# Kernel optimization log

Hardware: AMD Instinct MI355X
Metric: run time of the kernel (lower is better)

Reference implementation:

```python
import jax, jax.numpy as jnp
import numpy as np

N = 100000
E = 1600000
IN_DIM, HIDDEN, OUT_DIM, HEADS = 256, 128, 64, 2
NEG_SLOPE = 0.2


def setup_inputs() -> dict:
    key = jax.random.key(0)
    ks = jax.random.split(key, 10)
    inv = lambda d: 1.0 / np.sqrt(d)
    return {
        "x": jax.random.normal(ks[0], (N, IN_DIM), dtype=jnp.float32),
        "edge_index": jax.random.randint(ks[1], (2, E), 0, N, dtype=jnp.int64),
        "W1": jax.random.normal(ks[2], (IN_DIM, HEADS * HIDDEN), dtype=jnp.float32) * inv(IN_DIM),
        "att_src1": jax.random.normal(ks[3], (HEADS, HIDDEN), dtype=jnp.float32) * inv(HIDDEN),
        "att_dst1": jax.random.normal(ks[4], (HEADS, HIDDEN), dtype=jnp.float32) * inv(HIDDEN),
        "b1": jnp.zeros((HIDDEN,), dtype=jnp.float32),
        "W2": jax.random.normal(ks[5], (HIDDEN, OUT_DIM), dtype=jnp.float32) * inv(HIDDEN),
        "att_src2": jax.random.normal(ks[6], (1, OUT_DIM), dtype=jnp.float32) * inv(OUT_DIM),
        "att_dst2": jax.random.normal(ks[7], (1, OUT_DIM), dtype=jnp.float32) * inv(OUT_DIM),
        "b2": jnp.zeros((OUT_DIM,), dtype=jnp.float32),
    }


def gat_conv(x, W, att_src, att_dst, bias, src, dst, heads, ch):
    # Linear transform: [N, H, C]
    h = (x @ W).reshape(N, heads, ch)
    # Per-node attention logits: [N, H]
    a_s = jnp.einsum("nhc,hc->nh", h, att_src)
    a_d = jnp.einsum("nhc,hc->nh", h, att_dst)
    # Edge-wise scores (self-loops already in src/dst): [E', H]
    e = jax.nn.leaky_relu(a_s[src] + a_d[dst], NEG_SLOPE)
    # Segment softmax over incoming edges of each dst node
    m = jax.ops.segment_max(e, dst, num_segments=N)
    alpha = jnp.exp(e - m[dst])
    denom = jax.ops.segment_sum(alpha, dst, num_segments=N)
    alpha = alpha / denom[dst]
    # Weighted scatter-add aggregation: [N, H, C]
    out = jax.ops.segment_sum(alpha[:, :, None] * h[src], dst, num_segments=N)
    # concat=False -> mean over heads, then bias
    return out.mean(axis=1) + bias


def reference(x, edge_index, W1, att_src1, att_dst1, b1, W2, att_src2, att_dst2, b2):
    # PyG GATConv default: add self-loops
    loop = jnp.arange(N, dtype=edge_index.dtype)
    src = jnp.concatenate([edge_index[0], loop])
    dst = jnp.concatenate([edge_index[1], loop])
    h = gat_conv(x, W1, att_src1, att_dst1, b1, src, dst, HEADS, HIDDEN)
    h = jax.nn.relu(h)  # dropout is identity in eval mode
    out = gat_conv(h, W2, att_src2, att_dst2, b2, src, dst, 1, OUT_DIM)
    return out
```

## Files before the change

kernel.cpp:

```cpp
#include <hip/hip_runtime.h>
#include <hip/hip_bf16.h>
#include <cstdint>
#include <cstddef>

#define IN_D 256
#define HID 128
#define OUT_D 64
#define NSLOPE 0.2f
#define PAD 128
#define CSTR 16

typedef __attribute__((ext_vector_type(8))) short bf16x8;
typedef __attribute__((ext_vector_type(4))) float f32x4;
typedef __attribute__((ext_vector_type(8))) unsigned short u16x8;
typedef unsigned short u16;

static inline int cdiv(long long a, long long b) { return (int)((a + b - 1) / b); }

__device__ __forceinline__ float lrelu(float v) { return v >= 0.f ? v : NSLOPE * v; }

__device__ __forceinline__ u16 f2bf(float f) {
  unsigned u = __float_as_uint(f);
  return (u16)((u + 0x7FFFu + ((u >> 16) & 1u)) >> 16);
}
__device__ __forceinline__ float bf2f(u16 h) {
  return __uint_as_float((unsigned)h << 16);
}

__global__ void k_prep(const float* __restrict__ W1, u16* __restrict__ WThi,
                       u16* __restrict__ WTlo, const float* __restrict__ W2,
                       u16* __restrict__ W2Thi, u16* __restrict__ W2Tlo) {
  int idx = blockIdx.x * 256 + threadIdx.x;
  if (idx < IN_D * IN_D) {
    int k = idx >> 8, n = idx & 255;
    float f = W1[idx];
    u16 h = f2bf(f);
    WThi[n * IN_D + k] = h;
    WTlo[n * IN_D + k] = f2bf(f - bf2f(h));
  }
  int idx2 = idx - IN_D * IN_D;
  if (idx2 >= 0 && idx2 < HID * OUT_D) {
    int k = idx2 >> 6, n = idx2 & 63;
    float f = W2[idx2];
    u16 h = f2bf(f);
    W2Thi[n * HID + k] = h;
    W2Tlo[n * HID + k] = f2bf(f - bf2f(h));
  }
}

__launch_bounds__(512)
__global__ void k_gemm1buck(const float* __restrict__ x, const u16* __restrict__ WThi,
                            const u16* __restrict__ WTlo,
                            const float* __restrict__ as1, const float* __restrict__ ad1,
                            u16* __restrict__ hb, float* __restrict__ a_s,
                            float* __restrict__ a_d, int N,
                            const int* __restrict__ ei, int E,
                            int* __restrict__ cnt, int* __restrict__ colp,
                            int G1, int G2) {
  __shared__ u16 ldsb[2][10240];
  int bid = blockIdx.x;
  int m2 = (G1 < G2 ? G1 : G2) * 2;
  int type, tb;
  if (bid < m2) { type = bid & 1; tb = bid >> 1; }
  else { int ex = bid - m2; type = (G1 > G2) ? 0 : 1; tb = m2 / 2 + ex; }

  if (type == 1) {
    int base = tb * 2048 + threadIdx.x;
    int sv[4], dv[4]; bool vv[4];
    #pragma unroll
    for (int q = 0; q < 4; ++q) {
      int i = base + q * 512;
      vv[q] = i < E;
      int ic = vv[q] ? i : 0;
      sv[q] = ei[ic];
      dv[q] = ei[E + ic];
    }
    int pv[4];
    #pragma unroll
    for (int q = 0; q < 4; ++q)
      pv[q] = vv[q] ? atomicAdd(&cnt[(size_t)dv[q] * CSTR], 1) : PAD;
    #pragma unroll
    for (int q = 0; q < 4; ++q)
      if (pv[q] < PAD) colp[(size_t)dv[q] * PAD + pv[q]] = sv[q];
    return;
  }

  int tid = threadIdx.x;
  int w = tid >> 6, l = tid & 63;
  int l15 = l & 15, l4 = l >> 4;
  int rowbase = tb * 128 + w * 16;
  int row = rowbase + l15;
  int rowc = (row < N) ? row : (N - 1);
  const float* xp = x + (size_t)rowc * IN_D + l4 * 8;

  f32x4 acc[16];
  #pragma unroll
  for (int t = 0; t < 16; ++t) acc[t] = (f32x4){0.f, 0.f, 0.f, 0.f};

  const int ridx = (l15 * 5 + l4) * 8;

  for (int kk = 0; kk < 8; ++kk) {
    __syncthreads();
    #pragma unroll
    for (int it = 0; it < 2; ++it) {
      int c = tid + it * 512;
      int n = c >> 2, ch = c & 3;
      size_t soff = (size_t)n * IN_D + kk * 32 + ch * 8;
      uint4 vh = *(const uint4*)(WThi + soff);
      uint4 vl = *(const uint4*)(WTlo + soff);
      int dsl = (n * 5 + ch) * 8;
      *(uint4*)&ldsb[0][dsl] = vh;
      *(uint4*)&ldsb[1][dsl] = vl;
    }
    __syncthreads();

    f32x4 v0 = *(const f32x4*)(xp + kk * 32);
    f32x4 v1 = *(const f32x4*)(xp + kk * 32 + 4);
    bf16x8 ah, al;
    #pragma unroll
    for (int j = 0; j < 4; ++j) {
      u16 h0 = f2bf(v0[j]);
      ah[j] = (short)h0; al[j] = (short)f2bf(v0[j] - bf2f(h0));
      u16 h1 = f2bf(v1[j]);
      ah[j + 4] = (short)h1; al[j + 4] = (short)f2bf(v1[j] - bf2f(h1));
    }
    #pragma unroll
    for (int t = 0; t < 16; ++t) {
      bf16x8 bh = *(const bf16x8*)&ldsb[0][ridx + t * 640];
      bf16x8 bl = *(const bf16x8*)&ldsb[1][ridx + t * 640];
      acc[t] = __builtin_amdgcn_mfma_f32_16x16x32_bf16(ah, bh, acc[t], 0, 0, 0);
      acc[t] = __builtin_amdgcn_mfma_f32_16x16x32_bf16(al, bh, acc[t], 0, 0, 0);
      acc[t] = __builtin_amdgcn_mfma_f32_16x16x32_bf16(ah, bl, acc[t], 0, 0, 0);
    }
  }

  #pragma unroll
  for (int r = 0; r < 4; ++r) {
    int rr = rowbase + l4 * 4 + r;
    if (rr < N) {
      u16* hp = hb + (size_t)rr * IN_D + l15;
      #pragma unroll
      for (int t = 0; t < 16; ++t) hp[t * 16] = f2bf(acc[t][r]);
    }
  }
  float asv[16], adv[16];
  #pragma unroll
  for (int t = 0; t < 16; ++t) { asv[t] = as1[t * 16 + l15]; adv[t] = ad1[t * 16 + l15]; }
  float ps0[4] = {}, ps1[4] = {}, pd0[4] = {}, pd1[4] = {};
  #pragma unroll
  for (int t = 0; t < 16; ++t) {
    #pragma unroll
    for (int r = 0; r < 4; ++r) {
      float v = acc[t][r];
      if (t < 8) { ps0[r] += v * asv[t]; pd0[r] += v * adv[t]; }
      else       { ps1[r] += v * asv[t]; pd1[r] += v * adv[t]; }
    }
  }
  #pragma unroll
  for (int r = 0; r < 4; ++r) {
    #pragma unroll
    for (int o = 1; o < 16; o <<= 1) {
      ps0[r] += __shfl_xor(ps0[r], o); ps1[r] += __shfl_xor(ps1[r], o);
      pd0[r] += __shfl_xor(pd0[r], o); pd1[r] += __shfl_xor(pd1[r], o);
    }
    int rr = rowbase + l4 * 4 + r;
    if (l15 == 0 && rr < N) {
      a_s[rr * 2] = ps0[r]; a_s[rr * 2 + 1] = ps1[r];
      a_d[rr * 2] = pd0[r]; a_d[rr * 2 + 1] = pd1[r];
    }
  }
}

__launch_bounds__(256)
__global__ void k_fagg1(const int* __restrict__ cnt, const int* __restrict__ colp,
                        const float* __restrict__ a_s, const float* __restrict__ a_d,
                        const u16* __restrict__ hb, float* __restrict__ aggm, int N) {
  int gid = blockIdx.x * blockDim.x + threadIdx.x;
  int n = gid >> 6, lane = gid & 63;
  if (n >= N) return;
  size_t beg = (size_t)n * PAD;
  int cn = cnt[(size_t)n * CSTR]; cn = (cn < PAD) ? cn : PAD;
  float ad0 = a_d[2 * n], ad1 = a_d[2 * n + 1];

  int half = lane >> 5;
  int l5 = lane & 31;
  int head = l5 >> 4;
  float myAd = head ? ad1 : ad0;

  float sacc = 0.f;
  float accv[8] = {};
  if (half == 0) {
    float2 asn = *(const float2*)&a_s[2 * (size_t)n];
    float w = __expf(lrelu((head ? asn.y : asn.x) + myAd));
    sacc = w;
    const u16x8 hv = *(const u16x8*)&hb[(size_t)n * IN_D + l5 * 8];
    #pragma unroll
    for (int q = 0; q < 8; ++q) accv[q] = w * bf2f(hv[q]);
  }
  #pragma unroll 4
  for (int j = 0; j < cn; j += 2) {
    int jj = j + half;
    bool valid = jj < cn;
    int jc = valid ? jj : 0;
    int sidx = colp[beg + jc];
    float2 asv = *(const float2*)&a_s[2 * (size_t)sidx];
    float e = (head ? asv.y : asv.x) + myAd;
    float w = __expf(lrelu(e));
    w = valid ? w : 0.f;
    sacc += w;
    const u16x8 hv = *(const u16x8*)&hb[(size_t)sidx * IN_D + l5 * 8];
    #pragma unroll
    for (int q = 0; q < 8; ++q) accv[q] += w * bf2f(hv[q]);
  }
  sacc += __shfl_xor(sacc, 32);
  float myScale = 0.5f / sacc;
  #pragma unroll
  for (int q = 0; q < 8; ++q) {
    accv[q] *= myScale;
    accv[q] += __shfl_xor(accv[q], 16);
    accv[q] += __shfl_xor(accv[q], 32);
  }
  if (lane < 16) {
    float4 o0 = {accv[0], accv[1], accv[2], accv[3]};
    float4 o1 = {accv[4], accv[5], accv[6], accv[7]};
    *(float4*)&aggm[(size_t)n * HID + lane * 8] = o0;
    *(float4*)&aggm[(size_t)n * HID + lane * 8 + 4] = o1;
  }
}

__launch_bounds__(256)
__global__ void k_gemm2(const float* __restrict__ aggm, const float* __restrict__ b1,
                        const u16* __restrict__ WThi, const u16* __restrict__ WTlo,
                        const float* __restrict__ as2, const float* __restrict__ ad2,
                        u16* __restrict__ h2b, float* __restrict__ a_s,
                        float* __restrict__ a_d, int N) {
  int tid = threadIdx.x;
  int w = tid >> 6, l = tid & 63;
  int l15 = l & 15, l4 = l >> 4;
  int rowbase = blockIdx.x * 64 + w * 16;
  int row = rowbase + l15;
  int rowc = (row < N) ? row : (N - 1);
  const float* ap = aggm + (size_t)rowc * HID + l4 * 8;
  const float* bp = b1 + l4 * 8;

  f32x4 acc[4];
  #pragma unroll
  for (int t = 0; t < 4; ++t) acc[t] = (f32x4){0.f, 0.f, 0.f, 0.f};

  #pragma unroll
  for (int kk = 0; kk < 4; ++kk) {
    f32x4 v0 = *(const f32x4*)(ap + kk * 32);
    f32x4 v1 = *(const f32x4*)(ap + kk * 32 + 4);
    f32x4 b0 = *(const f32x4*)(bp + kk * 32);
    f32x4 b1v = *(const f32x4*)(bp + kk * 32 + 4);
    bf16x8 ah, al;
    #pragma unroll
    for (int j = 0; j < 4; ++j) {
      float u0 = v0[j] + b0[j]; u0 = (u0 > 0.f) ? u0 : 0.f;
      u16 h0 = f2bf(u0);
      ah[j] = (short)h0; al[j] = (short)f2bf(u0 - bf2f(h0));
      float u1 = v1[j] + b1v[j]; u1 = (u1 > 0.f) ? u1 : 0.f;
      u16 h1 = f2bf(u1);
      ah[j + 4] = (short)h1; al[j + 4] = (short)f2bf(u1 - bf2f(h1));
    }
    size_t boff = (size_t)l15 * HID + kk * 32 + l4 * 8;
    #pragma unroll
    for (int t = 0; t < 4; ++t) {
      bf16x8 bh = *(const bf16x8*)(WThi + boff + (size_t)t * 16 * HID);
      bf16x8 bl = *(const bf16x8*)(WTlo + boff + (size_t)t * 16 * HID);
      acc[t] = __builtin_amdgcn_mfma_f32_16x16x32_bf16(ah, bh, acc[t], 0, 0, 0);
      acc[t] = __builtin_amdgcn_mfma_f32_16x16x32_bf16(al, bh, acc[t], 0, 0, 0);
      acc[t] = __builtin_amdgcn_mfma_f32_16x16x32_bf16(ah, bl, acc[t], 0, 0, 0);
    }
  }

  #pragma unroll
  for (int r = 0; r < 4; ++r) {
    int rr = rowbase + l4 * 4 + r;
    if (rr < N) {
      u16* hp = h2b + (size_t)rr * OUT_D + l15;
      #pragma unroll
      for (int t = 0; t < 4; ++t) hp[t * 16] = f2bf(acc[t][r]);
    }
  }
  float asv[4], adv[4];
  #pragma unroll
  for (int t = 0; t < 4; ++t) { asv[t] = as2[t * 16 + l15]; adv[t] = ad2[t * 16 + l15]; }
  #pragma unroll
  for (int r = 0; r < 4; ++r) {
    float ps = 0.f, pd = 0.f;
    #pragma unroll
    for (int t = 0; t < 4; ++t) { ps += acc[t][r] * asv[t]; pd += acc[t][r] * adv[t]; }
    #pragma unroll
    for (int o = 1; o < 16; o <<= 1) { ps += __shfl_xor(ps, o); pd += __shfl_xor(pd, o); }
    int rr = rowbase + l4 * 4 + r;
    if (l15 == 0 && rr < N) { a_s[rr] = ps; a_d[rr] = pd; }
  }
}

__launch_bounds__(256)
__global__ void k_fagg2(const int* __restrict__ cnt, const int* __restrict__ colp,
                        const float* __restrict__ a_s, const float* __restrict__ a_d,
                        const u16* __restrict__ h2b, const float* __restrict__ b2,
                        float* __restrict__ out, int N) {
  int gid = blockIdx.x * blockDim.x + threadIdx.x;
  int n = gid >> 6, lane = gid & 63;
  if (n >= N) return;
  size_t beg = (size_t)n * PAD;
  int cn = cnt[(size_t)n * CSTR]; cn = (cn < PAD) ? cn : PAD;
  float ad = a_d[n];

  int g = lane >> 3, l3 = lane & 7;
  float sacc = 0.f;
  float accv[8] = {};
  if (g == 0) {
    float w = __expf(lrelu(a_s[n] + ad));
    sacc = w;
    const u16x8 hv = *(const u16x8*)&h2b[(size_t)n * OUT_D + l3 * 8];
    #pragma unroll
    for (int q = 0; q < 8; ++q) accv[q] = w * bf2f(hv[q]);
  }
  #pragma unroll 4
  for (int j = 0; j < cn; j += 8) {
    int jj = j + g;
    bool valid = jj < cn;
    int jc = valid ? jj : 0;
    int sidx = colp[beg + jc];
    float w = __expf(lrelu(a_s[sidx] + ad));
    w = valid ? w : 0.f;
    sacc += w;
    const u16x8 hv = *(const u16x8*)&h2b[(size_t)sidx * OUT_D + l3 * 8];
    #pragma unroll
    for (int q = 0; q < 8; ++q) accv[q] += w * bf2f(hv[q]);
  }
  sacc += __shfl_xor(sacc, 8);
  sacc += __shfl_xor(sacc, 16);
  sacc += __shfl_xor(sacc, 32);
  float rcp = 1.f / sacc;
  #pragma unroll
  for (int q = 0; q < 8; ++q) {
    accv[q] *= rcp;
    accv[q] += __shfl_xor(accv[q], 8);
    accv[q] += __shfl_xor(accv[q], 16);
    accv[q] += __shfl_xor(accv[q], 32);
  }
  if (lane < 8) {
    float* op = out + (size_t)n * OUT_D + lane * 8;
    const float* bp = b2 + lane * 8;
    float4 o0 = {accv[0] + bp[0], accv[1] + bp[1], accv[2] + bp[2], accv[3] + bp[3]};
    float4 o1 = {accv[4] + bp[4], accv[5] + bp[5], accv[6] + bp[6], accv[7] + bp[7]};
    *(float4*)op = o0;
    *(float4*)(op + 4) = o1;
  }
}

extern "C" void kernel_launch(void* const* d_in, const int* in_sizes, int n_in,
                              void* d_out, int out_size, void* d_ws, size_t ws_size,
                              hipStream_t stream) {
  const float* x    = (const float*)d_in[0];
  const int*   ei   = (const int*)d_in[1];
  const float* W1   = (const float*)d_in[2];
  const float* as1w = (const float*)d_in[3];
  const float* ad1w = (const float*)d_in[4];
  const float* b1   = (const float*)d_in[5];
  const float* W2   = (const float*)d_in[6];
  const float* as2w = (const float*)d_in[7];
  const float* ad2w = (const float*)d_in[8];
  const float* b2   = (const float*)d_in[9];
  float* out = (float*)d_out;

  const int N  = in_sizes[0] / IN_D;
  const int E  = in_sizes[1] / 2;

  float* ws = (float*)d_ws;
  size_t off = 0;
  u16*   hb1  = (u16*)(ws + off); off += (size_t)N * IN_D / 2;
  u16*   h2b  = (u16*)(ws + off); off += (size_t)N * OUT_D / 2;
  float* aggm = ws + off; off += (size_t)N * HID;
  float* a_s1 = ws + off; off += (size_t)N * 2;
  float* a_d1 = ws + off; off += (size_t)N * 2;
  float* a_s2 = ws + off; off += N;
  float* a_d2 = ws + off; off += N;
  int*   cnt  = (int*)(ws + off); off += (size_t)N * CSTR;
  int*   colp = (int*)(ws + off); off += (size_t)N * PAD;
  u16*   WThi = (u16*)(ws + off); off += (IN_D * IN_D) / 2;
  u16*   WTlo = (u16*)(ws + off); off += (IN_D * IN_D) / 2;
  u16*   W2Thi = (u16*)(ws + off); off += (HID * OUT_D) / 2;
  u16*   W2Tlo = (u16*)(ws + off); off += (HID * OUT_D) / 2;

  hipMemsetAsync(cnt, 0, (size_t)N * CSTR * sizeof(int), stream);

  k_prep<<<cdiv(IN_D * IN_D + HID * OUT_D, 256), 256, 0, stream>>>(
      W1, WThi, WTlo, W2, W2Thi, W2Tlo);

  const int G1 = cdiv(N, 128);
  const int G2 = cdiv(E, 2048);
  k_gemm1buck<<<G1 + G2, 512, 0, stream>>>(x, WThi, WTlo, as1w, ad1w, hb1, a_s1, a_d1, N,
                                           ei, E, cnt, colp, G1, G2);

  k_fagg1<<<cdiv((long long)N * 64, 256), 256, 0, stream>>>(cnt, colp, a_s1, a_d1, hb1, aggm, N);

  k_gemm2<<<cdiv(N, 64), 256, 0, stream>>>(aggm, b1, W2Thi, W2Tlo, as2w, ad2w, h2b, a_s2, a_d2, N);
  k_fagg2<<<cdiv((long long)N * 64, 256), 256, 0, stream>>>(cnt, colp, a_s2, a_d2, h2b, b2, out, N);
}
```

Baseline: 374.5 us.

## Fuse layer-1 aggregation with layer-2 GEMM and compact degree counters

```diff
diff --git a/kernel.cpp b/kernel.cpp
--- a/kernel.cpp
+++ b/kernel.cpp
@@ -8,7 +8,6 @@
 #define OUT_D 64
 #define NSLOPE 0.2f
 #define PAD 128
-#define CSTR 16
 
 typedef __attribute__((ext_vector_type(8))) short bf16x8;
 typedef __attribute__((ext_vector_type(4))) float f32x4;
@@ -78,7 +77,7 @@
     int pv[4];
     #pragma unroll
     for (int q = 0; q < 4; ++q)
-      pv[q] = vv[q] ? atomicAdd(&cnt[(size_t)dv[q] * CSTR], 1) : PAD;
+      pv[q] = vv[q] ? atomicAdd(&cnt[dv[q]], 1) : PAD;
     #pragma unroll
     for (int q = 0; q < 4; ++q)
       if (pv[q] < PAD) colp[(size_t)dv[q] * PAD + pv[q]] = sv[q];
@@ -172,129 +171,116 @@
 }
 
 __launch_bounds__(256)
-__global__ void k_fagg1(const int* __restrict__ cnt, const int* __restrict__ colp,
-                        const float* __restrict__ a_s, const float* __restrict__ a_d,
-                        const u16* __restrict__ hb, float* __restrict__ aggm, int N) {
-  int gid = blockIdx.x * blockDim.x + threadIdx.x;
-  int n = gid >> 6, lane = gid & 63;
-  if (n >= N) return;
-  size_t beg = (size_t)n * PAD;
-  int cn = cnt[(size_t)n * CSTR]; cn = (cn < PAD) ? cn : PAD;
-  float ad0 = a_d[2 * n], ad1 = a_d[2 * n + 1];
+__global__ void k_fagg1g2(const int* __restrict__ cnt, const int* __restrict__ colp,
+                          const float* __restrict__ a_s, const float* __restrict__ a_d,
+                          const u16* __restrict__ hb, const float* __restrict__ b1,
+                          const u16* __restrict__ W2Thi, const u16* __restrict__ W2Tlo,
+                          const float* __restrict__ as2, const float* __restrict__ ad2,
+                          u16* __restrict__ h2b, float* __restrict__ a_s2,
+                          float* __restrict__ a_d2, int N) {
+  __shared__ float rowLds[16][132];
+  __shared__ float red[2][16][4];
+  int tid = threadIdx.x;
+  int wid = tid >> 6, lane = tid & 63;
+  int base = blockIdx.x * 16;
 
   int half = lane >> 5;
   int l5 = lane & 31;
   int head = l5 >> 4;
-  float myAd = head ? ad1 : ad0;
-
-  float sacc = 0.f;
-  float accv[8] = {};
-  if (half == 0) {
-    float2 asn = *(const float2*)&a_s[2 * (size_t)n];
-    float w = __expf(lrelu((head ? asn.y : asn.x) + myAd));
-    sacc = w;
-    const u16x8 hv = *(const u16x8*)&hb[(size_t)n * IN_D + l5 * 8];
-    #pragma unroll
-    for (int q = 0; q < 8; ++q) accv[q] = w * bf2f(hv[q]);
-  }
-  #pragma unroll 4
-  for (int j = 0; j < cn; j += 2) {
-    int jj = j + half;
-    bool valid = jj < cn;
-    int jc = valid ? jj : 0;
-    int sidx = colp[beg + jc];
-    float2 asv = *(const float2*)&a_s[2 * (size_t)sidx];
-    float e = (head ? asv.y : asv.x) + myAd;
-    float w = __expf(lrelu(e));
-    w = valid ? w : 0.f;
-    sacc += w;
-    const u16x8 hv = *(const u16x8*)&hb[(size_t)sidx * IN_D + l5 * 8];
-    #pragma unroll
-    for (int q = 0; q < 8; ++q) accv[q] += w * bf2f(hv[q]);
-  }
-  sacc += __shfl_xor(sacc, 32);
-  float myScale = 0.5f / sacc;
-  #pragma unroll
-  for (int q = 0; q < 8; ++q) {
-    accv[q] *= myScale;
-    accv[q] += __shfl_xor(accv[q], 16);
-    accv[q] += __shfl_xor(accv[q], 32);
-  }
-  if (lane < 16) {
-    float4 o0 = {accv[0], accv[1], accv[2], accv[3]};
-    float4 o1 = {accv[4], accv[5], accv[6], accv[7]};
-    *(float4*)&aggm[(size_t)n * HID + lane * 8] = o0;
-    *(float4*)&aggm[(size_t)n * HID + lane * 8 + 4] = o1;
-  }
-}
-
-__launch_bounds__(256)
-__global__ void k_gemm2(const float* __restrict__ aggm, const float* __restrict__ b1,
-                        const u16* __restrict__ WThi, const u16* __restrict__ WTlo,
-                        const float* __restrict__ as2, const float* __restrict__ ad2,
-                        u16* __restrict__ h2b, float* __restrict__ a_s,
-                        float* __restrict__ a_d, int N) {
-  int tid = threadIdx.x;
-  int w = tid >> 6, l = tid & 63;
-  int l15 = l & 15, l4 = l >> 4;
-  int rowbase = blockIdx.x * 64 + w * 16;
-  int row = rowbase + l15;
-  int rowc = (row < N) ? row : (N - 1);
-  const float* ap = aggm + (size_t)rowc * HID + l4 * 8;
-  const float* bp = b1 + l4 * 8;
-
-  f32x4 acc[4];
-  #pragma unroll
-  for (int t = 0; t < 4; ++t) acc[t] = (f32x4){0.f, 0.f, 0.f, 0.f};
-
+
+  for (int rr = 0; rr < 4; ++rr) {
+    int ln = wid * 4 + rr;
+    int n = base + ln;
+    if (n >= N) { if (lane < 16) for (int q = 0; q < 8; ++q) rowLds[ln][lane * 8 + q] = 0.f; continue; }
+    size_t begb = (size_t)n * PAD;
+    int cn = cnt[n]; cn = (cn < PAD) ? cn : PAD;
+    float ad0 = a_d[2 * n], ad1 = a_d[2 * n + 1];
+    float myAd = head ? ad1 : ad0;
+
+    float sacc = 0.f;
+    float accv[8] = {};
+    if (half == 0) {
+      float2 asn = *(const float2*)&a_s[2 * (size_t)n];
+      float wv = __expf(lrelu((head ? asn.y : asn.x) + myAd));
+      sacc = wv;
+      const u16x8 hv = *(const u16x8*)&hb[(size_t)n * IN_D + l5 * 8];
+      #pragma unroll
+      for (int q = 0; q < 8; ++q) accv[q] = wv * bf2f(hv[q]);
+    }
+    #pragma unroll 4
+    for (int j = 0; j < cn; j += 2) {
+      int jj = j + half;
+      bool valid = jj < cn;
+      int jc = valid ? jj : 0;
+      int sidx = colp[begb + jc];
+      float2 asv = *(const float2*)&a_s[2 * (size_t)sidx];
+      float e = (head ? asv.y : asv.x) + myAd;
+      float wv = __expf(lrelu(e));
+      wv = valid ? wv : 0.f;
+      sacc += wv;
+      const u16x8 hv = *(const u16x8*)&hb[(size_t)sidx * IN_D + l5 * 8];
+      #pragma unroll
+      for (int q = 0; q < 8; ++q) accv[q] += wv * bf2f(hv[q]);
+    }
+    sacc += __shfl_xor(sacc, 32);
+    float myScale = 0.5f / sacc;
+    #pragma unroll
+    for (int q = 0; q < 8; ++q) {
+      accv[q] *= myScale;
+      accv[q] += __shfl_xor(accv[q], 16);
+      accv[q] += __shfl_xor(accv[q], 32);
+    }
+    if (lane < 16) {
+      #pragma unroll
+      for (int q = 0; q < 8; ++q) rowLds[ln][lane * 8 + q] = accv[q];
+    }
+  }
+  __syncthreads();
+
+  int l15 = lane & 15, l4 = lane >> 4;
+  f32x4 acc2 = (f32x4){0.f, 0.f, 0.f, 0.f};
   #pragma unroll
   for (int kk = 0; kk < 4; ++kk) {
-    f32x4 v0 = *(const f32x4*)(ap + kk * 32);
-    f32x4 v1 = *(const f32x4*)(ap + kk * 32 + 4);
-    f32x4 b0 = *(const f32x4*)(bp + kk * 32);
-    f32x4 b1v = *(const f32x4*)(bp + kk * 32 + 4);
+    int k0 = kk * 32 + l4 * 8;
+    f32x4 bv0 = *(const f32x4*)(b1 + k0);
+    f32x4 bv1 = *(const f32x4*)(b1 + k0 + 4);
     bf16x8 ah, al;
     #pragma unroll
     for (int j = 0; j < 4; ++j) {
-      float u0 = v0[j] + b0[j]; u0 = (u0 > 0.f) ? u0 : 0.f;
+      float u0 = rowLds[l15][k0 + j] + bv0[j]; u0 = (u0 > 0.f) ? u0 : 0.f;
       u16 h0 = f2bf(u0);
       ah[j] = (short)h0; al[j] = (short)f2bf(u0 - bf2f(h0));
-      float u1 = v1[j] + b1v[j]; u1 = (u1 > 0.f) ? u1 : 0.f;
+      float u1 = rowLds[l15][k0 + 4 + j] + bv1[j]; u1 = (u1 > 0.f) ? u1 : 0.f;
       u16 h1 = f2bf(u1);
       ah[j + 4] = (short)h1; al[j + 4] = (short)f2bf(u1 - bf2f(h1));
     }
-    size_t boff = (size_t)l15 * HID + kk * 32 + l4 * 8;
-    #pragma unroll
-    for (int t = 0; t < 4; ++t) {
-      bf16x8 bh = *(const bf16x8*)(WThi + boff + (size_t)t * 16 * HID);
-      bf16x8 bl = *(const bf16x8*)(WTlo + boff + (size_t)t * 16 * HID);
-      acc[t] = __builtin_amdgcn_mfma_f32_16x16x32_bf16(ah, bh, acc[t], 0, 0, 0);
-      acc[t] = __builtin_amdgcn_mfma_f32_16x16x32_bf16(al, bh, acc[t], 0, 0, 0);
-      acc[t] = __builtin_amdgcn_mfma_f32_16x16x32_bf16(ah, bl, acc[t], 0, 0, 0);
-    }
-  }
-
+    size_t boff = (size_t)(wid * 16 + l15) * HID + k0;
+    bf16x8 bh = *(const bf16x8*)(W2Thi + boff);
+    bf16x8 bl = *(const bf16x8*)(W2Tlo + boff);
+    acc2 = __builtin_amdgcn_mfma_f32_16x16x32_bf16(ah, bh, acc2, 0, 0, 0);
+    acc2 = __builtin_amdgcn_mfma_f32_16x16x32_bf16(al, bh, acc2, 0, 0, 0);
+    acc2 = __builtin_amdgcn_mfma_f32_16x16x32_bf16(ah, bl, acc2, 0, 0, 0);
+  }
+
+  float asv = as2[wid * 16 + l15], adv = ad2[wid * 16 + l15];
+  float ps[4], pd[4];
   #pragma unroll
   for (int r = 0; r < 4; ++r) {
-    int rr = rowbase + l4 * 4 + r;
-    if (rr < N) {
-      u16* hp = h2b + (size_t)rr * OUT_D + l15;
-      #pragma unroll
-      for (int t = 0; t < 4; ++t) hp[t * 16] = f2bf(acc[t][r]);
-    }
-  }
-  float asv[4], adv[4];
-  #pragma unroll
-  for (int t = 0; t < 4; ++t) { asv[t] = as2[t * 16 + l15]; adv[t] = ad2[t * 16 + l15]; }
-  #pragma unroll
-  for (int r = 0; r < 4; ++r) {
-    float ps = 0.f, pd = 0.f;
-    #pragma unroll
-    for (int t = 0; t < 4; ++t) { ps += acc[t][r] * asv[t]; pd += acc[t][r] * adv[t]; }
-    #pragma unroll
-    for (int o = 1; o < 16; o <<= 1) { ps += __shfl_xor(ps, o); pd += __shfl_xor(pd, o); }
-    int rr = rowbase + l4 * 4 + r;
-    if (l15 == 0 && rr < N) { a_s[rr] = ps; a_d[rr] = pd; }
+    int n = base + l4 * 4 + r;
+    if (n < N) h2b[(size_t)n * OUT_D + wid * 16 + l15] = f2bf(acc2[r]);
+    ps[r] = acc2[r] * asv; pd[r] = acc2[r] * adv;
+    #pragma unroll
+    for (int o = 1; o < 16; o <<= 1) { ps[r] += __shfl_xor(ps[r], o); pd[r] += __shfl_xor(pd[r], o); }
+    if (l15 == 0) { red[0][l4 * 4 + r][wid] = ps[r]; red[1][l4 * 4 + r][wid] = pd[r]; }
+  }
+  __syncthreads();
+  if (tid < 32) {
+    int ln = tid >> 1, kind = tid & 1;
+    int n = base + ln;
+    if (n < N) {
+      float v = red[kind][ln][0] + red[kind][ln][1] + red[kind][ln][2] + red[kind][ln][3];
+      if (kind == 0) a_s2[n] = v; else a_d2[n] = v;
+    }
   }
 }
 
@@ -307,7 +293,7 @@
   int n = gid >> 6, lane = gid & 63;
   if (n >= N) return;
   size_t beg = (size_t)n * PAD;
-  int cn = cnt[(size_t)n * CSTR]; cn = (cn < PAD) ? cn : PAD;
+  int cn = cnt[n]; cn = (cn < PAD) ? cn : PAD;
   float ad = a_d[n];
 
   int g = lane >> 3, l3 = lane & 7;
@@ -376,19 +362,18 @@
   size_t off = 0;
   u16*   hb1  = (u16*)(ws + off); off += (size_t)N * IN_D / 2;
   u16*   h2b  = (u16*)(ws + off); off += (size_t)N * OUT_D / 2;
-  float* aggm = ws + off; off += (size_t)N * HID;
   float* a_s1 = ws + off; off += (size_t)N * 2;
   float* a_d1 = ws + off; off += (size_t)N * 2;
   float* a_s2 = ws + off; off += N;
   float* a_d2 = ws + off; off += N;
-  int*   cnt  = (int*)(ws + off); off += (size_t)N * CSTR;
+  int*   cnt  = (int*)(ws + off); off += N;
   int*   colp = (int*)(ws + off); off += (size_t)N * PAD;
   u16*   WThi = (u16*)(ws + off); off += (IN_D * IN_D) / 2;
   u16*   WTlo = (u16*)(ws + off); off += (IN_D * IN_D) / 2;
   u16*   W2Thi = (u16*)(ws + off); off += (HID * OUT_D) / 2;
   u16*   W2Tlo = (u16*)(ws + off); off += (HID * OUT_D) / 2;
 
-  hipMemsetAsync(cnt, 0, (size_t)N * CSTR * sizeof(int), stream);
+  hipMemsetAsync(cnt, 0, (size_t)N * sizeof(int), stream);
 
   k_prep<<<cdiv(IN_D * IN_D + HID * OUT_D, 256), 256, 0, stream>>>(
       W1, WThi, WTlo, W2, W2Thi, W2Tlo);
@@ -398,8 +383,8 @@
   k_gemm1buck<<<G1 + G2, 512, 0, stream>>>(x, WThi, WTlo, as1w, ad1w, hb1, a_s1, a_d1, N,
                                            ei, E, cnt, colp, G1, G2);
 
-  k_fagg1<<<cdiv((long long)N * 64, 256), 256, 0, stream>>>(cnt, colp, a_s1, a_d1, hb1, aggm, N);
-
-  k_gemm2<<<cdiv(N, 64), 256, 0, stream>>>(aggm, b1, W2Thi, W2Tlo, as2w, ad2w, h2b, a_s2, a_d2, N);
+  k_fagg1g2<<<cdiv(N, 16), 256, 0, stream>>>(cnt, colp, a_s1, a_d1, hb1, b1,
+                                             W2Thi, W2Tlo, as2w, ad2w, h2b, a_s2, a_d2, N);
+
   k_fagg2<<<cdiv((long long)N * 64, 256), 256, 0, stream>>>(cnt, colp, a_s2, a_d2, h2b, b2, out, N);
 }
```

After: 329.6 us. 1.14x faster.
